# Performance work log

Hardware: AMD Instinct MI355X
Metric: run time of the kernel (lower is better)

Reference implementation:

```python
import jax, jax.numpy as jnp
import numpy as np

B, S, A, C, M, CE = 2, 8, 24000, 80, 20, 7
POS_TH, NEG_TH = 0.5, 0.4
V0, V1 = 0.1, 0.2              # SSD encode variances
SL1_BETA = 1.0 / 9.0
ALPHA, GAMMA = 0.25, 2.0
CB_BETA = 0.9999
EPS = 1e-7


def point_form(cf):
    # (cx,cy,w,h) -> (x1,y1,x2,y2)
    return jnp.concatenate([cf[..., :2] - cf[..., 2:] * 0.5, cf[..., :2] + cf[..., 2:] * 0.5], -1)


def jaccard(a, b):
    # a: [M,4], b: [A,4] point form -> IoU [M,A]
    lt = jnp.maximum(a[:, None, :2], b[None, :, :2])
    rb = jnp.minimum(a[:, None, 2:], b[None, :, 2:])
    wh = jnp.clip(rb - lt, 0.0)
    inter = wh[..., 0] * wh[..., 1]
    aa = (a[:, 2] - a[:, 0]) * (a[:, 3] - a[:, 1])
    ab = (b[:, 2] - b[:, 0]) * (b[:, 3] - b[:, 1])
    return inter / (aa[:, None] + ab[None, :] - inter + 1e-10)


def encode(matched, anchors_cf):
    # matched: [A,4] point form gt, anchors_cf: [A,4] center form
    g_cxcy = ((matched[:, :2] + matched[:, 2:]) * 0.5 - anchors_cf[:, :2]) / (V0 * anchors_cf[:, 2:])
    g_wh = jnp.log(jnp.clip(matched[:, 2:] - matched[:, :2], 1e-6) / anchors_cf[:, 2:]) / V1
    return jnp.concatenate([g_cxcy, g_wh], -1)


def bce(p, y):
    p = jnp.clip(p, EPS, 1.0 - EPS)
    return -(y * jnp.log(p) + (1.0 - y) * jnp.log1p(-p))


def match_one(gtb, gtl, count, anchors_pf, anchors_cf):
    # SSD-style match with ignore band: conf in {-1 ignore, 0 background, i+1 positive matched to gt i}
    valid = jnp.arange(M) < count
    iou = jnp.where(valid[:, None], jaccard(gtb, anchors_pf), -1.0)  # [M,A]
    best_prior_idx = jnp.argmax(iou, axis=1)                         # best anchor per gt
    best_truth_iou = jnp.max(iou, axis=0)                            # best gt per anchor
    best_truth_idx = jnp.argmax(iou, axis=0)
    sidx = jnp.where(valid, best_prior_idx, A)                       # out-of-range -> dropped
    best_truth_iou = best_truth_iou.at[sidx].set(2.0, mode='drop')   # force each gt's best anchor positive
    best_truth_idx = best_truth_idx.at[sidx].set(jnp.arange(M), mode='drop')
    conf = (best_truth_idx + 1).astype(jnp.int32)                    # dummy labels = gt index
    conf = jnp.where(best_truth_iou < POS_TH, -1, conf)
    conf = jnp.where(best_truth_iou < NEG_TH, 0, conf)
    loc = encode(gtb[best_truth_idx], anchors_cf)
    has = count > 0
    conf = jnp.where(has, conf, -1)                                  # empty frame -> all ignore
    loc = jnp.where(has, loc, 0.0)
    # gather per-anchor multi-hot labels: labels_bs = [zeros; gt_labels][dumy_conf]
    lab = jnp.where((conf > 0)[:, None], gtl[jnp.clip(conf - 1, 0, M - 1)], 0.0)
    return conf, loc, lab


def setup_inputs() -> dict:
    key = jax.random.key(0)
    ks = jax.random.split(key, 10)
    confidence = jax.random.normal(ks[0], (B, S, A, C), jnp.float32)
    predicted_locations = jax.random.normal(ks[1], (B, S, A, 4), jnp.float32)
    gc = jax.random.uniform(ks[2], (B, S, M, 2))
    gw = jax.random.uniform(ks[3], (B, S, M, 2), minval=0.05, maxval=0.4)
    gt_boxes = jnp.clip(jnp.concatenate([gc - gw * 0.5, gc + gw * 0.5], -1), 0.0, 1.0)
    gt_labels = (jax.random.uniform(ks[4], (B, S, M, C)) < 0.05).astype(jnp.float32)
    counts = jax.random.randint(ks[5], (B, S), 0, M + 1, jnp.int32)
    ac = jax.random.uniform(ks[6], (A, 2))
    aw = jax.random.uniform(ks[7], (A, 2), minval=0.02, maxval=0.3)
    anchors = jnp.concatenate([ac, aw], -1)  # center form (cx,cy,w,h)
    ego_preds = jax.random.normal(ks[8], (B, S, CE), jnp.float32)
    ego_labels = jax.random.randint(ks[9], (B, S), 0, CE, jnp.int32)
    cls_num_list = jax.random.randint(jax.random.fold_in(key, 11), (C,), 1, 10000, jnp.int32)
    return {"confidence": confidence, "predicted_locations": predicted_locations,
            "gt_boxes": gt_boxes, "gt_labels": gt_labels, "counts": counts,
            "anchors": anchors, "ego_preds": ego_preds, "ego_labels": ego_labels,
            "cls_num_list": cls_num_list}


def reference(confidence, predicted_locations, gt_boxes, gt_labels, counts, anchors, ego_preds, ego_labels, cls_num_list):
    preds = jax.nn.sigmoid(confidence)
    anchors_pf = point_form(anchors)
    flat = lambda x: x.reshape((B * S,) + x.shape[2:])
    conf_t, loc_t, lab_t = jax.vmap(match_one, in_axes=(0, 0, 0, None, None))(
        flat(gt_boxes), flat(gt_labels), counts.reshape(-1), anchors_pf, anchors)
    labels_bin = jax.lax.stop_gradient(conf_t.reshape(B, S, A).astype(jnp.float32))
    gt_locations = jax.lax.stop_gradient(loc_t.reshape(B, S, A, 4))
    all_labels = jax.lax.stop_gradient(lab_t.reshape(B, S, A, C))

    pos = (labels_bin > 0).astype(jnp.float32)
    num_pos = jnp.maximum(1.0, pos.sum())
    n = jnp.abs(predicted_locations - gt_locations)
    sl1 = jnp.where(n < SL1_BETA, 0.5 * n * n / SL1_BETA, n - 0.5 * SL1_BETA)
    regression_loss = (sl1 * pos[..., None]).sum() / (num_pos * 4.0)

    # class-balanced focal loss (module hardcodes gamma=1 inside sigmoid_cb_focal_loss)
    cmask = (labels_bin > -1).astype(jnp.float32)[..., None]
    w = (1.0 - CB_BETA) / (1.0 - jnp.power(jnp.float32(CB_BETA), cls_num_list.astype(jnp.float32)))
    w = w / w.sum()
    y = all_labels
    pt = preds * y + (1.0 - preds) * (1.0 - y)
    cb = w * y + (1.0 - CB_BETA) * (1.0 - y)
    cls_loss = (bce(preds, y) * cb * (1.0 - pt) * cmask).sum() / num_pos

    # ego focal loss (replicates original get_one_hot_labels column semantics)
    ep = jax.nn.sigmoid(ego_preds)
    evalid = ego_labels > -1
    col = (jnp.where(evalid[..., None], jax.nn.one_hot(ego_labels, CE), 0.0).sum((0, 1)) > 0).astype(jnp.float32)
    oh = jnp.broadcast_to(col, ep.shape)
    af = ALPHA * oh + (1.0 - ALPHA) * (1.0 - oh)
    ept = ep * oh + (1.0 - ep) * (1.0 - oh)
    n_ego = evalid.sum().astype(jnp.float32)
    ego_sum = (bce(ep, oh) * af * (1.0 - ept) ** GAMMA * evalid[..., None].astype(jnp.float32)).sum()
    ego_loss = jnp.where(n_ego > 0, ego_sum / jnp.maximum(n_ego, 1.0), 0.0)

    return regression_loss, cls_loss / 8.0 + ego_loss / 4.0
```

## Files before the change

### kernel.cpp

```cpp
#include <hip/hip_runtime.h>
#include <math.h>

#define NB 2
#define NS 8
#define NA 24000
#define NC 80
#define NM 20
#define NCE 7
#define NBS (NB*NS)
#define CPB 75
#define APC (NA/CPB)

#define POS_TH 0.5f
#define NEG_TH 0.4f
#define OMB 1e-4f

__device__ inline unsigned long long packKey(float f, unsigned idx) {
    unsigned u = __float_as_uint(f);
    u = (u & 0x80000000u) ? ~u : (u | 0x80000000u);
    return ((unsigned long long)u << 32) | (unsigned long long)(0xFFFFFFFFu - idx);
}

typedef float v4f __attribute__((ext_vector_type(4)));
__device__ inline float4 ntload4(const float4* p) {
    v4f v = __builtin_nontemporal_load((const v4f*)p);
    return make_float4(v.x, v.y, v.z, v.w);
}

__global__ void __launch_bounds__(256)
k_gbest(const float* __restrict__ gtb, const int* __restrict__ counts,
        const float* __restrict__ anchors, unsigned long long* __restrict__ gbest) {
    int bid = blockIdx.x;
    int bs = bid / CPB;
    int chunk = bid % CPB;
    int t = threadIdx.x;
    int cnt = counts[bs];
    if (cnt == 0) return;

    __shared__ float sg[NM][5];
    if (t < NM) {
        const float* g = gtb + ((size_t)bs * NM + t) * 4;
        float x1 = g[0], y1 = g[1], x2 = g[2], y2 = g[3];
        sg[t][0] = x1; sg[t][1] = y1; sg[t][2] = x2; sg[t][3] = y2;
        sg[t][4] = (x2 - x1) * (y2 - y1);
    }
    __syncthreads();

    int a0 = chunk * APC;
    bool has2 = t < (APC - 256);
    float4 c1 = ((const float4*)anchors)[a0 + t];
    float bx1 = c1.x - c1.z * 0.5f, by1 = c1.y - c1.w * 0.5f;
    float bx2 = c1.x + c1.z * 0.5f, by2 = c1.y + c1.w * 0.5f;
    float bar = (bx2 - bx1) * (by2 - by1);
    float cx1 = 0, cy1 = 0, cx2 = 0, cy2 = 0, car = 0;
    if (has2) {
        float4 c2 = ((const float4*)anchors)[a0 + 256 + t];
        cx1 = c2.x - c2.z * 0.5f; cy1 = c2.y - c2.w * 0.5f;
        cx2 = c2.x + c2.z * 0.5f; cy2 = c2.y + c2.w * 0.5f;
        car = (cx2 - cx1) * (cy2 - cy1);
    }

    __shared__ unsigned long long sk[4][NM];
    int wave = t >> 6, lane = t & 63;
    for (int m = 0; m < cnt; m++) {
        float gx1 = sg[m][0], gy1 = sg[m][1], gx2 = sg[m][2], gy2 = sg[m][3], gar = sg[m][4];
        float ltx = fmaxf(gx1, bx1), lty = fmaxf(gy1, by1);
        float rbx = fminf(gx2, bx2), rby = fminf(gy2, by2);
        float wx = fmaxf(rbx - ltx, 0.0f), wy = fmaxf(rby - lty, 0.0f);
        float inter = wx * wy;
        float iou = inter / (gar + bar - inter + 1e-10f);
        unsigned long long k = packKey(iou, (unsigned)(a0 + t));
        if (has2) {
            float ltx2 = fmaxf(gx1, cx1), lty2 = fmaxf(gy1, cy1);
            float rbx2 = fminf(gx2, cx2), rby2 = fminf(gy2, cy2);
            float wx2 = fmaxf(rbx2 - ltx2, 0.0f), wy2 = fmaxf(rby2 - lty2, 0.0f);
            float inter2 = wx2 * wy2;
            float iou2 = inter2 / (gar + car - inter2 + 1e-10f);
            unsigned long long k2 = packKey(iou2, (unsigned)(a0 + 256 + t));
            if (k2 > k) k = k2;
        }
        #pragma unroll
        for (int off = 32; off > 0; off >>= 1) {
            unsigned long long o = __shfl_xor(k, off);
            if (o > k) k = o;
        }
        if (lane == 0) sk[wave][m] = k;
    }
    __syncthreads();
    if (t < cnt) {
        unsigned long long k = sk[0][t];
        if (sk[1][t] > k) k = sk[1][t];
        if (sk[2][t] > k) k = sk[2][t];
        if (sk[3][t] > k) k = sk[3][t];
        atomicMax(&gbest[bs * NM + t], k);
    }
}

__global__ void __launch_bounds__(256, 5)
k_match(const float* __restrict__ gtb, const int* __restrict__ counts,
        const float* __restrict__ anchors, const float* __restrict__ ploc,
        const float* __restrict__ gtl, const float* __restrict__ logits,
        const int* __restrict__ cls_num,
        const unsigned long long* __restrict__ gbest,
        double* __restrict__ acc, int* __restrict__ npos) {
    int bid = blockIdx.x;
    int bs = bid / CPB;
    int chunk = bid % CPB;
    int t = threadIdx.x;
    int cnt = counts[bs];

    __shared__ float sg[NM][5];
    __shared__ unsigned abest[NM];
    __shared__ float wsh[NC];
    __shared__ float wsum_sh;
    __shared__ float smask[APC];
    __shared__ unsigned qpos[APC];
    __shared__ int npq;
    if (t == 0) npq = 0;
    if (t < NM) {
        const float* g = gtb + ((size_t)bs * NM + t) * 4;
        float x1 = g[0], y1 = g[1], x2 = g[2], y2 = g[3];
        sg[t][0] = x1; sg[t][1] = y1; sg[t][2] = x2; sg[t][3] = y2;
        sg[t][4] = (x2 - x1) * (y2 - y1);
        if (t < cnt)
            abest[t] = 0xFFFFFFFFu - (unsigned)(gbest[bs * NM + t] & 0xFFFFFFFFull);
    }
    if (t < NC) {
        float n = (float)cls_num[t];
        wsh[t] = OMB / (1.0f - powf(0.9999f, n));
    }
    __syncthreads();
    if (t == 0) {
        float s = 0.0f;
        for (int c = 0; c < NC; c++) s += wsh[c];
        wsum_sh = s;
    }
    __syncthreads();
    if (t < NC) wsh[t] = wsh[t] / wsum_sh;

    const float SL1B = 1.0f / 9.0f;
    float regsum = 0.0f;
    int pcnt = 0;
    int a0 = chunk * APC;
    for (int al = t; al < APC; al += 256) {
        int a = a0 + al;
        float4 cf = ((const float4*)anchors)[a];
        float ax1 = cf.x - cf.z * 0.5f, ay1 = cf.y - cf.w * 0.5f;
        float ax2 = cf.x + cf.z * 0.5f, ay2 = cf.y + cf.w * 0.5f;
        float aarea = (ax2 - ax1) * (ay2 - ay1);
        float best = -1.0f; int bm = 0;
        for (int m = 0; m < cnt; m++) {
            float ltx = fmaxf(sg[m][0], ax1), lty = fmaxf(sg[m][1], ay1);
            float rbx = fminf(sg[m][2], ax2), rby = fminf(sg[m][3], ay2);
            float wx = fmaxf(rbx - ltx, 0.0f), wy = fmaxf(rby - lty, 0.0f);
            float inter = wx * wy;
            float iou = inter / (sg[m][4] + aarea - inter + 1e-10f);
            if (iou > best) { best = iou; bm = m; }
        }
        for (int m = 0; m < cnt; m++) {
            if (abest[m] == (unsigned)a) { best = 2.0f; bm = m; }
        }
        int code;
        if (cnt == 0) code = -1;
        else if (best < NEG_TH) code = 0;
        else if (best < POS_TH) code = -1;
        else code = bm + 1;
        smask[al] = (code == -1) ? 0.0f : 1.0f;
        if (code > 0) {
            pcnt++;
            size_t ia = (size_t)bs * NA + a;
            float mx1 = sg[bm][0], my1 = sg[bm][1], mx2 = sg[bm][2], my2 = sg[bm][3];
            float g0 = ((mx1 + mx2) * 0.5f - cf.x) / (0.1f * cf.z);
            float g1 = ((my1 + my2) * 0.5f - cf.y) / (0.1f * cf.w);
            float g2 = logf(fmaxf(mx2 - mx1, 1e-6f) / cf.z) / 0.2f;
            float g3 = logf(fmaxf(my2 - my1, 1e-6f) / cf.w) / 0.2f;
            float4 p = ((const float4*)ploc)[ia];
            float n0 = fabsf(p.x - g0), n1 = fabsf(p.y - g1);
            float n2 = fabsf(p.z - g2), n3 = fabsf(p.w - g3);
            float s0 = n0 < SL1B ? 0.5f * n0 * n0 / SL1B : n0 - 0.5f * SL1B;
            float s1 = n1 < SL1B ? 0.5f * n1 * n1 / SL1B : n1 - 0.5f * SL1B;
            float s2 = n2 < SL1B ? 0.5f * n2 * n2 / SL1B : n2 - 0.5f * SL1B;
            float s3 = n3 < SL1B ? 0.5f * n3 * n3 / SL1B : n3 - 0.5f * SL1B;
            regsum += s0 + s1 + s2 + s3;
            int q = atomicAdd(&npq, 1);
            qpos[q] = ((unsigned)bm << 16) | (unsigned)al;
        }
    }
    __syncthreads();

    const float4* x4p = (const float4*)logits + ((size_t)bs * NA + a0) * (NC / 4);
    float bgsum = 0.0f;
    #pragma unroll
    for (int g = 0; g < 5; g++) {
        float4 xs[5];
        float  ms[5];
        #pragma unroll
        for (int j = 0; j < 5; j++) {
            int i = t + (g * 5 + j) * 256;
            ms[j] = smask[i / 20];
            xs[j] = ntload4(&x4p[i]);
        }
        #pragma unroll
        for (int j = 0; j < 5; j++) {
            float xv[4] = {xs[j].x, xs[j].y, xs[j].z, xs[j].w};
            float tsum = 0.0f;
            #pragma unroll
            for (int jj = 0; jj < 4; jj++) {
                float x = xv[jj];
                float e = __expf(-x);
                float s = 1.0f + e;
                float pr = __builtin_amdgcn_rcpf(s);
                float ls = __logf(s);
                tsum += (x + ls) * pr;
            }
            bgsum = fmaf(ms[j], tsum, bgsum);
        }
    }

    float corrsum = 0.0f;
    int nq = npq;
    for (int i = t; i < nq * 20; i += 256) {
        int qq = i / 20, c4 = i % 20;
        unsigned e = qpos[qq];
        int al = e & 0xFFFFu;
        int m  = (int)(e >> 16);
        float4 y4 = ((const float4*)(gtl + ((size_t)(bs * NM + m)) * NC))[c4];
        if (y4.x > 0.5f || y4.y > 0.5f || y4.z > 0.5f || y4.w > 0.5f) {
            float4 x4 = ((const float4*)(logits + ((size_t)bs * NA + a0 + al) * NC))[c4];
            float yv[4] = {y4.x, y4.y, y4.z, y4.w};
            float xv[4] = {x4.x, x4.y, x4.z, x4.w};
            #pragma unroll
            for (int j = 0; j < 4; j++) {
                if (yv[j] > 0.5f) {
                    float x = xv[j];
                    float ee = __expf(-x);
                    float s = 1.0f + ee;
                    float pr = __builtin_amdgcn_rcpf(s);
                    float ls = __logf(s);
                    corrsum += ls * wsh[c4 * 4 + j] * (ee * pr)
                             - OMB * (x + ls) * pr;
                }
            }
        }
    }
    float clssum = corrsum + OMB * bgsum;

    #pragma unroll
    for (int off = 32; off > 0; off >>= 1) {
        regsum += __shfl_xor(regsum, off);
        clssum += __shfl_xor(clssum, off);
        pcnt   += __shfl_xor(pcnt, off);
    }
    __shared__ float sf[4], sc[4];
    __shared__ int   si[4];
    int wave = t >> 6, lane = t & 63;
    if (lane == 0) { sf[wave] = regsum; sc[wave] = clssum; si[wave] = pcnt; }
    __syncthreads();
    if (t == 0) {
        atomicAdd(&acc[0], (double)(sf[0] + sf[1] + sf[2] + sf[3]));
        atomicAdd(&acc[1], (double)(sc[0] + sc[1] + sc[2] + sc[3]));
        atomicAdd(npos, si[0] + si[1] + si[2] + si[3]);
    }
}

__global__ void k_final(const float* __restrict__ ego_preds, const int* __restrict__ ego_labels,
                        const double* __restrict__ acc, const int* __restrict__ npos,
                        float* __restrict__ out) {
    __shared__ float scol[NCE];
    __shared__ float sred[128];
    __shared__ int   sval[128];
    const float EPSF = 1e-7f;
    int t = threadIdx.x;
    if (t < NCE) {
        float c = 0.0f;
        for (int i = 0; i < NBS; i++) {
            int l = ego_labels[i];
            if (l > -1 && l == t) c = 1.0f;
        }
        scol[t] = c;
    }
    __syncthreads();

    float term = 0.0f;
    if (t < NBS * NCE) {
        int bs = t / NCE, e = t % NCE;
        int lbl = ego_labels[bs];
        if (lbl > -1) {
            float x = ego_preds[t];
            float ep = 1.0f / (1.0f + expf(-x));
            float oh = scol[e];
            float af = 0.25f * oh + 0.75f * (1.0f - oh);
            float ept = ep * oh + (1.0f - ep) * (1.0f - oh);
            float epc = fminf(fmaxf(ep, EPSF), 1.0f - EPSF);
            float bce = -(oh * logf(epc) + (1.0f - oh) * log1pf(-epc));
            float om = 1.0f - ept;
            term = bce * af * om * om;
        }
    }
    sred[t] = term;
    sval[t] = (t < NBS && ego_labels[t] > -1) ? 1 : 0;
    __syncthreads();
    for (int off = 64; off > 0; off >>= 1) {
        if (t < off) { sred[t] += sred[t + off]; sval[t] += sval[t + off]; }
        __syncthreads();
    }
    if (t == 0) {
        float esum = sred[0];
        int ne = sval[0];
        float ego = (ne > 0) ? esum / (float)(ne > 1 ? ne : 1) : 0.0f;
        double npd = (double)(*npos);
        if (npd < 1.0) npd = 1.0;
        out[0] = (float)(acc[0] / (npd * 4.0));
        out[1] = (float)(acc[1] / npd / 8.0 + (double)ego / 4.0);
    }
}

extern "C" void kernel_launch(void* const* d_in, const int* in_sizes, int n_in,
                              void* d_out, int out_size, void* d_ws, size_t ws_size,
                              hipStream_t stream) {
    const float* confidence = (const float*)d_in[0];
    const float* ploc       = (const float*)d_in[1];
    const float* gtb        = (const float*)d_in[2];
    const float* gtl        = (const float*)d_in[3];
    const int*   counts     = (const int*)d_in[4];
    const float* anchors    = (const float*)d_in[5];
    const float* ego_preds  = (const float*)d_in[6];
    const int*   ego_labels = (const int*)d_in[7];
    const int*   cls_num    = (const int*)d_in[8];
    float* out = (float*)d_out;

    char* ws = (char*)d_ws;
    double* acc  = (double*)ws;
    int* npos    = (int*)(ws + 16);
    unsigned long long* gbest = (unsigned long long*)(ws + 64);

    hipMemsetAsync(ws, 0, 4096, stream);
    k_gbest<<<NBS * CPB, 256, 0, stream>>>(gtb, counts, anchors, gbest);
    k_match<<<NBS * CPB, 256, 0, stream>>>(gtb, counts, anchors, ploc, gtl, confidence,
                                           cls_num, gbest, acc, npos);
    k_final<<<1, 128, 0, stream>>>(ego_preds, ego_labels, acc, npos, out);
}
```

Measured before the change: 275.6 us.

## Split background focal-loss streaming into separate wide kernel via global mask

Moves the dense per-logit background loss pass out of the matching kernel into a new kernel launched with 3000 blocks. The matching kernel now writes the per-anchor ignore mask to global workspace instead of shared memory. The aim is more parallelism and better memory-bandwidth saturation on the roughly 123 MB logits stream, which the original 1200-block grid limited. The cost is an extra launch plus a global round trip for the mask.

```diff
diff --git a/kernel.cpp b/kernel.cpp
--- a/kernel.cpp
+++ b/kernel.cpp
@@ -14,6 +14,9 @@
 #define POS_TH 0.5f
 #define NEG_TH 0.4f
 #define OMB 1e-4f
+
+#define CLS_BLOCKS 3000
+#define CLS_F4_PER_BLOCK 2560
 
 __device__ inline unsigned long long packKey(float f, unsigned idx) {
     unsigned u = __float_as_uint(f);
@@ -96,12 +99,13 @@
     }
 }
 
-__global__ void __launch_bounds__(256, 5)
+__global__ void __launch_bounds__(256)
 k_match(const float* __restrict__ gtb, const int* __restrict__ counts,
         const float* __restrict__ anchors, const float* __restrict__ ploc,
         const float* __restrict__ gtl, const float* __restrict__ logits,
         const int* __restrict__ cls_num,
         const unsigned long long* __restrict__ gbest,
+        float* __restrict__ maskG,
         double* __restrict__ acc, int* __restrict__ npos) {
     int bid = blockIdx.x;
     int bs = bid / CPB;
@@ -113,7 +117,6 @@
     __shared__ unsigned abest[NM];
     __shared__ float wsh[NC];
     __shared__ float wsum_sh;
-    __shared__ float smask[APC];
     __shared__ unsigned qpos[APC];
     __shared__ int npq;
     if (t == 0) npq = 0;
@@ -165,7 +168,7 @@
         else if (best < NEG_TH) code = 0;
         else if (best < POS_TH) code = -1;
         else code = bm + 1;
-        smask[al] = (code == -1) ? 0.0f : 1.0f;
+        maskG[(size_t)bs * NA + a] = (code == -1) ? 0.0f : 1.0f;
         if (code > 0) {
             pcnt++;
             size_t ia = (size_t)bs * NA + a;
@@ -187,35 +190,6 @@
         }
     }
     __syncthreads();
-
-    const float4* x4p = (const float4*)logits + ((size_t)bs * NA + a0) * (NC / 4);
-    float bgsum = 0.0f;
-    #pragma unroll
-    for (int g = 0; g < 5; g++) {
-        float4 xs[5];
-        float  ms[5];
-        #pragma unroll
-        for (int j = 0; j < 5; j++) {
-            int i = t + (g * 5 + j) * 256;
-            ms[j] = smask[i / 20];
-            xs[j] = ntload4(&x4p[i]);
-        }
-        #pragma unroll
-        for (int j = 0; j < 5; j++) {
-            float xv[4] = {xs[j].x, xs[j].y, xs[j].z, xs[j].w};
-            float tsum = 0.0f;
-            #pragma unroll
-            for (int jj = 0; jj < 4; jj++) {
-                float x = xv[jj];
-                float e = __expf(-x);
-                float s = 1.0f + e;
-                float pr = __builtin_amdgcn_rcpf(s);
-                float ls = __logf(s);
-                tsum += (x + ls) * pr;
-            }
-            bgsum = fmaf(ms[j], tsum, bgsum);
-        }
-    }
 
     float corrsum = 0.0f;
     int nq = npq;
@@ -243,24 +217,64 @@
             }
         }
     }
-    float clssum = corrsum + OMB * bgsum;
 
     #pragma unroll
     for (int off = 32; off > 0; off >>= 1) {
-        regsum += __shfl_xor(regsum, off);
-        clssum += __shfl_xor(clssum, off);
-        pcnt   += __shfl_xor(pcnt, off);
+        regsum  += __shfl_xor(regsum, off);
+        corrsum += __shfl_xor(corrsum, off);
+        pcnt    += __shfl_xor(pcnt, off);
     }
     __shared__ float sf[4], sc[4];
     __shared__ int   si[4];
     int wave = t >> 6, lane = t & 63;
-    if (lane == 0) { sf[wave] = regsum; sc[wave] = clssum; si[wave] = pcnt; }
+    if (lane == 0) { sf[wave] = regsum; sc[wave] = corrsum; si[wave] = pcnt; }
     __syncthreads();
     if (t == 0) {
         atomicAdd(&acc[0], (double)(sf[0] + sf[1] + sf[2] + sf[3]));
         atomicAdd(&acc[1], (double)(sc[0] + sc[1] + sc[2] + sc[3]));
         atomicAdd(npos, si[0] + si[1] + si[2] + si[3]);
     }
+}
+
+__global__ void __launch_bounds__(256, 4)
+k_cls(const float* __restrict__ logits, const float* __restrict__ maskG,
+      double* __restrict__ acc) {
+    int t = threadIdx.x;
+    unsigned f40 = (unsigned)blockIdx.x * CLS_F4_PER_BLOCK + (unsigned)t;
+    const float4* x4p = (const float4*)logits;
+
+    float4 xs[10];
+    float  ms[10];
+    #pragma unroll
+    for (int k = 0; k < 10; k++) {
+        unsigned i = f40 + (unsigned)(k * 256);
+        ms[k] = maskG[i / 20u];
+        xs[k] = ntload4(&x4p[i]);
+    }
+    float bgsum = 0.0f;
+    #pragma unroll
+    for (int k = 0; k < 10; k++) {
+        float xv[4] = {xs[k].x, xs[k].y, xs[k].z, xs[k].w};
+        float tsum = 0.0f;
+        #pragma unroll
+        for (int jj = 0; jj < 4; jj++) {
+            float x = xv[jj];
+            float e = __expf(-x);
+            float s = 1.0f + e;
+            float pr = __builtin_amdgcn_rcpf(s);
+            float ls = __logf(s);
+            tsum += (x + ls) * pr;
+        }
+        bgsum = fmaf(ms[k], tsum, bgsum);
+    }
+
+    #pragma unroll
+    for (int off = 32; off > 0; off >>= 1) bgsum += __shfl_xor(bgsum, off);
+    __shared__ float sb[4];
+    int wave = t >> 6, lane = t & 63;
+    if (lane == 0) sb[wave] = bgsum;
+    __syncthreads();
+    if (t == 0) atomicAdd(&acc[1], (double)(OMB * (sb[0] + sb[1] + sb[2] + sb[3])));
 }
 
 __global__ void k_final(const float* __restrict__ ego_preds, const int* __restrict__ ego_labels,
@@ -333,10 +347,12 @@
     double* acc  = (double*)ws;
     int* npos    = (int*)(ws + 16);
     unsigned long long* gbest = (unsigned long long*)(ws + 64);
+    float* maskG = (float*)(ws + 4096);
 
     hipMemsetAsync(ws, 0, 4096, stream);
     k_gbest<<<NBS * CPB, 256, 0, stream>>>(gtb, counts, anchors, gbest);
     k_match<<<NBS * CPB, 256, 0, stream>>>(gtb, counts, anchors, ploc, gtl, confidence,
-                                           cls_num, gbest, acc, npos);
+                                           cls_num, gbest, maskG, acc, npos);
+    k_cls<<<CLS_BLOCKS, 256, 0, stream>>>(confidence, maskG, acc);
     k_final<<<1, 128, 0, stream>>>(ego_preds, ego_labels, acc, npos, out);
 }
```

Result: no change. 276.6 us (+0.4%).
